# Kernel optimization log

Measured on AMD Instinct MI355X. Metric: run time of the kernel, lower is better.

## Reference

```python
import jax, jax.numpy as jnp
import numpy as np

B, T_IN, T_OUT, R = 32, 128, 500, 5
MEM_D, ATT, DEC, MEL, SPEC = 256, 256, 256, 128, 513
SPK_N, SPK_D = 5, 32
N_STYLE, STYLE_D, STYLE_ATT = 10, 2, 2
STEPS = T_OUT // R


def _gru(x, h, Wg, bg, Wc, bc):
    # TF GRUCell: r,u gates then candidate with reset-gated state
    gates = jax.nn.sigmoid(jnp.concatenate([x, h], -1) @ Wg + bg)
    r, u = jnp.split(gates, 2, axis=-1)
    c = jnp.tanh(jnp.concatenate([x, r * h], -1) @ Wc + bc)
    return u * h + (1.0 - u) * c


def setup_inputs() -> dict:
    key = jax.random.key(0)
    ks = iter(jax.random.split(key, 48))
    def nrm(shape, s=0.05):
        return (jax.random.normal(next(ks), shape) * s).astype(jnp.float32)
    return dict(
        encoder_output=nrm((B, T_IN, MEM_D), 1.0),
        style_token=nrm((N_STYLE, STYLE_D), 1.0),
        mel_gtruth=nrm((B, T_OUT, MEL), 1.0),
        speaker=jax.random.randint(next(ks), (B,), 0, SPK_N),
        inp_mask=jax.random.randint(next(ks), (B,), T_IN // 2, T_IN + 1),
        spk_embed=nrm((SPK_N, SPK_D)),
        Wp1=nrm((MEL, 256)), bp1=jnp.zeros((256,), jnp.float32),
        Wp2=nrm((256, 128)), bp2=jnp.zeros((128,), jnp.float32),
        Wg_att=nrm((128 + SPK_D + ATT, 2 * ATT)), bg_att=jnp.ones((2 * ATT,), jnp.float32),
        Wc_att=nrm((128 + SPK_D + ATT, ATT)), bc_att=jnp.zeros((ATT,), jnp.float32),
        Wk=nrm((MEM_D, ATT)), Wq=nrm((ATT, ATT)), v_att=nrm((ATT,)),
        Ws_pre=nrm((STYLE_D, STYLE_D)), bs_pre=jnp.zeros((STYLE_D,), jnp.float32),
        Wk_s=nrm((STYLE_D, STYLE_ATT)), Wq_s=nrm((ATT, STYLE_ATT)), v_s=nrm((STYLE_ATT,)),
        Wa=nrm((ATT + SPK_D + MEM_D + STYLE_D, DEC)), ba=jnp.zeros((DEC,), jnp.float32),
        Wg1=nrm((2 * DEC, 2 * DEC)), bg1=jnp.ones((2 * DEC,), jnp.float32),
        Wc1=nrm((2 * DEC, DEC)), bc1=jnp.zeros((DEC,), jnp.float32),
        Wg2=nrm((2 * DEC, 2 * DEC)), bg2=jnp.ones((2 * DEC,), jnp.float32),
        Wc2=nrm((2 * DEC, DEC)), bc2=jnp.zeros((DEC,), jnp.float32),
        Wo=nrm((DEC, MEL * R)), bo=jnp.zeros((MEL * R,), jnp.float32),
        Wspec=nrm((MEL, SPEC)), bspec=jnp.zeros((SPEC,), jnp.float32),
    )


def reference(encoder_output, style_token, mel_gtruth, speaker, inp_mask, spk_embed,
              Wp1, bp1, Wp2, bp2, Wg_att, bg_att, Wc_att, bc_att,
              Wk, Wq, v_att, Ws_pre, bs_pre, Wk_s, Wq_s, v_s,
              Wa, ba, Wg1, bg1, Wc1, bc1, Wg2, bg2, Wc2, bc2,
              Wo, bo, Wspec, bspec):
    mask = jnp.arange(T_IN)[None, :] < inp_mask[:, None]          # [B, T_in]
    keys = encoder_output @ Wk                                     # precomputed attention keys [B,T_in,ATT]
    spk = spk_embed[speaker]                                       # [B, 32]
    mem_style = jax.nn.relu(style_token @ Ws_pre + bs_pre)         # style pre-net [10, 2]
    keys_s = mem_style @ Wk_s                                      # [10, 2]
    # teacher forcing: frame fed at step t is indic[r*t + r - 1] = last gt frame of previous group
    mel_t = jnp.transpose(mel_gtruth, (1, 0, 2))                   # [T_out, B, MEL]
    last = mel_t[R - 1::R]                                         # [STEPS, B, MEL]
    prev = jnp.concatenate([jnp.zeros((1, B, MEL), mel_gtruth.dtype), last[:-1]], 0)

    def step(carry, frame):
        h_att, h1, h2 = carry
        # decoder pre-net (dropout disabled: is_training=False)
        p = jax.nn.relu(frame @ Wp1 + bp1)
        p = jax.nn.relu(p @ Wp2 + bp2)
        h_att = _gru(jnp.concatenate([p, spk], -1), h_att, Wg_att, bg_att, Wc_att, bc_att)
        q = h_att
        # content attention (Bahdanau) over encoder memory
        e = jnp.einsum('bta,a->bt', jnp.tanh(keys + (q @ Wq)[:, None, :]), v_att)
        alpha = jax.nn.softmax(jnp.where(mask, e, -1e9), axis=-1)
        context = jnp.einsum('bt,btd->bd', alpha, encoder_output)
        # style attention over 10 style tokens
        e_s = jnp.einsum('bna,a->bn', jnp.tanh(keys_s[None, :, :] + (q @ Wq_s)[:, None, :]), v_s)
        alpha_s = jax.nn.softmax(e_s, axis=-1)
        context_s = alpha_s @ mem_style                            # [B, 2]
        aco_in = jnp.concatenate([h_att, spk, context, context_s], -1) @ Wa + ba
        # two residual-wrapped GRU layers
        h1n = _gru(aco_in, h1, Wg1, bg1, Wc1, bc1)
        y1 = h1n + aco_in
        h2n = _gru(y1, h2, Wg2, bg2, Wc2, bc2)
        y2 = h2n + y1
        return (h_att, h1n, h2n), (y2 @ Wo + bo, alpha)

    init = (jnp.zeros((B, ATT), jnp.float32),
            jnp.zeros((B, DEC), jnp.float32),
            jnp.zeros((B, DEC), jnp.float32))
    _, (outs, alphas) = jax.lax.scan(step, init, prev)
    output_mel = jnp.transpose(outs, (1, 0, 2)).reshape(B, T_OUT, MEL)
    output_spec = output_mel @ Wspec + bspec
    final_alpha = jnp.transpose(alphas, (1, 0, 2))                 # [B, STEPS, T_in]
    return output_mel, output_spec, final_alpha
```

## Files before the change

### kernel.cpp

```cpp
#include <hip/hip_runtime.h>

typedef unsigned short ushort_t;
typedef unsigned int   uint_t;
typedef unsigned long long u64;
typedef __attribute__((ext_vector_type(8))) short  bf16x8;
typedef __attribute__((ext_vector_type(4))) float  f32x4;

#define B_      32
#define TIN_    128
#define TOUT_   500
#define R_      5
#define STEPS_  100
#define MEL_    128
#define SPEC_   513
#define NWG_    32

#define ZB_SLOTS   0
#define ZB_AH      8192
#define ZB_ARH     24576
#define ZB_AHC     40960
#define ZB_AXH1    73728
#define ZB_AXRH1   106496
#define ZB_AY1H2   139264
#define ZB_AY1RH2  172032
#define ZB_UBUF    221184
#define ZB_U1BUF   253952
#define ZB_U2BUF   286720
#define ZB_QSBUF   335872
#define ZB_END     435200
#define OFF_ACOSPK2 505856
#define OFF_MS2     538624
#define OFF_KS2     539136
#define OFF_SPK2    501760
#define OFF_PREG2   539648
#define OFF_PREC2   7093248
#define OFF_Y2G     10370048
#define OFF_KEYSP   13646848
#define OFF_ENCP    15744000
#define OFF_WQB     17841152

__device__ __forceinline__ float bf1(ushort_t u){ return __uint_as_float(((uint_t)u) << 16); }
__device__ __forceinline__ ushort_t f2bf(float f){
    uint_t b = __float_as_uint(f);
    uint_t r = (b + 0x7fffu + ((b >> 16) & 1u)) >> 16;
    return (ushort_t)r;
}
__device__ __forceinline__ float fexp2(float x){ return __builtin_amdgcn_exp2f(x); }
__device__ __forceinline__ float frcp(float x){ return __builtin_amdgcn_rcpf(x); }
__device__ __forceinline__ float sigm_f(float x){ return frcp(1.f + fexp2(-1.44269504f * x)); }
__device__ __forceinline__ float tanh_f(float x){
    float e = fexp2(2.88539008f * x);
    return 1.f - 2.f * frcp(e + 1.f);
}
__device__ __forceinline__ u64 ld8(const void* p){
    return __hip_atomic_load((const u64*)p, __ATOMIC_RELAXED, __HIP_MEMORY_SCOPE_AGENT);
}
__device__ __forceinline__ void st8(void* p, u64 v){
    __hip_atomic_store((u64*)p, v, __ATOMIC_RELAXED, __HIP_MEMORY_SCOPE_AGENT);
}
__device__ __forceinline__ float ld4f(const void* p){
    uint_t u = __hip_atomic_load((const uint_t*)p, __ATOMIC_RELAXED, __HIP_MEMORY_SCOPE_AGENT);
    return __uint_as_float(u);
}
__device__ __forceinline__ void st4f(void* p, float v){
    __hip_atomic_store((uint_t*)p, __float_as_uint(v), __ATOMIC_RELAXED, __HIP_MEMORY_SCOPE_AGENT);
}
__device__ __forceinline__ float u64lo(u64 v){ return __uint_as_float((uint_t)v); }
__device__ __forceinline__ float u64hi(u64 v){ return __uint_as_float((uint_t)(v >> 32)); }
__device__ __forceinline__ u64 pack4(const ushort_t* q){
    return (u64)q[0] | ((u64)q[1] << 16) | ((u64)q[2] << 32) | ((u64)q[3] << 48);
}
__device__ __forceinline__ u64 pack2f(const float* f){
    return (u64)__float_as_uint(f[0]) | ((u64)__float_as_uint(f[1]) << 32);
}
#define CBAR() asm volatile("" ::: "memory")

__global__ __launch_bounds__(256) void k_small(
    const float* __restrict__ st, const float* __restrict__ Ws_pre,
    const float* __restrict__ bs_pre, const float* __restrict__ Wk_s,
    const float* __restrict__ spk_embed, const int* __restrict__ speaker,
    const float* __restrict__ Wa, const float* __restrict__ ba,
    float* __restrict__ spk_sel, float* __restrict__ aco_spk,
    float* __restrict__ ms_g, float* __restrict__ ks_g)
{
    __shared__ float spk_l[B_*32];
    __shared__ float ms_l[20];
    const int tid = threadIdx.x;
    for(int i=tid; i<B_*32; i+=256){
        int b = i >> 5, j = i & 31;
        float v = spk_embed[speaker[b]*32 + j];
        spk_l[i] = v; spk_sel[i] = v;
    }
    if(tid < 20){
        int n = tid >> 1, j = tid & 1;
        float v = st[n*2]*Ws_pre[j] + st[n*2+1]*Ws_pre[2+j] + bs_pre[j];
        v = fmaxf(v, 0.f);
        ms_l[tid] = v; ms_g[tid] = v;
    }
    __syncthreads();
    if(tid < 20){
        int n = tid >> 1, j = tid & 1;
        ks_g[tid] = ms_l[n*2]*Wk_s[j] + ms_l[n*2+1]*Wk_s[2+j];
    }
    for(int i=tid; i<B_*256; i+=256){
        int b = i >> 8, n = i & 255;
        float acc = ba[n];
        #pragma unroll
        for(int k=0;k<32;++k) acc = fmaf(spk_l[b*32+k], Wa[(256+k)*256 + n], acc);
        aco_spk[i] = acc;
    }
}

__global__ __launch_bounds__(256) void k_keys(const float* __restrict__ enc,
                                              const float* __restrict__ Wk,
                                              ushort_t* __restrict__ keysb){
    __shared__ float x16[16][256];
    const int bid = blockIdx.x;
    const int b = bid >> 3, tg = bid & 7, t0 = tg*16;
    const int tid = threadIdx.x;
    for(int i=tid; i<16*256; i+=256){
        int r = i >> 8, k = i & 255;
        x16[r][k] = enc[((size_t)b*TIN_ + t0 + r)*256 + k];
    }
    __syncthreads();
    float acc[16];
    #pragma unroll
    for(int r=0;r<16;++r) acc[r] = 0.f;
    for(int k=0;k<256;++k){
        float w = Wk[k*256 + tid];
        #pragma unroll
        for(int r=0;r<16;++r) acc[r] = fmaf(x16[r][k], w, acc[r]);
    }
    #pragma unroll
    for(int r=0;r<16;++r)
        keysb[((size_t)b*TIN_ + t0 + r)*256 + tid] = f2bf(acc[r]);
}

__global__ __launch_bounds__(256) void k_cvt_enc(const float* __restrict__ enc,
                                                 ushort_t* __restrict__ encb){
    int o = blockIdx.x*256 + threadIdx.x;
    encb[o] = f2bf(enc[o]);
}
__global__ __launch_bounds__(256) void k_cvt_wq(const float* __restrict__ Wq,
                                                ushort_t* __restrict__ wqT){
    int o = blockIdx.x*256 + threadIdx.x;
    int k = o >> 8, c = o & 255;
    wqT[(k>>3)*2048 + c*8 + (k&7)] = f2bf(Wq[k*256 + c]);
}

__global__ __launch_bounds__(256) void k_prenet(
    const float* __restrict__ mg, const float* __restrict__ spk_sel,
    const float* __restrict__ Wp1, const float* __restrict__ bp1,
    const float* __restrict__ Wp2, const float* __restrict__ bp2,
    const float* __restrict__ Wg_att, const float* __restrict__ bg_att,
    const float* __restrict__ Wc_att, const float* __restrict__ bc_att,
    float* __restrict__ preg, float* __restrict__ prec)
{
    __shared__ float fr[16][128];
    __shared__ float p1[16][256];
    __shared__ float p2[16][128];
    __shared__ float spk_l[16][32];
    const int r0 = blockIdx.x * 16;
    const int tid = threadIdx.x;
    for(int i=tid; i<16*128; i+=256){
        int r = i >> 7, mcol = i & 127;
        int row = r0 + r, s = row >> 5, b = row & 31;
        fr[r][mcol] = (s == 0) ? 0.f : mg[((size_t)b*TOUT_ + s*R_ - 1)*MEL_ + mcol];
    }
    for(int i=tid; i<16*32; i+=256){
        int r = i >> 5, j = i & 31;
        spk_l[r][j] = spk_sel[((r0 + r) & 31)*32 + j];
    }
    __syncthreads();
    {
        float acc[16];
        #pragma unroll
        for(int r=0;r<16;++r) acc[r]=0.f;
        for(int k=0;k<128;++k){
            float w = Wp1[k*256 + tid];
            #pragma unroll
            for(int r=0;r<16;++r) acc[r] = fmaf(fr[r][k], w, acc[r]);
        }
        float bb = bp1[tid];
        #pragma unroll
        for(int r=0;r<16;++r) p1[r][tid] = fmaxf(acc[r] + bb, 0.f);
    }
    __syncthreads();
    if(tid < 128){
        float acc[16];
        #pragma unroll
        for(int r=0;r<16;++r) acc[r]=0.f;
        for(int k=0;k<256;++k){
            float w = Wp2[k*128 + tid];
            #pragma unroll
            for(int r=0;r<16;++r) acc[r] = fmaf(p1[r][k], w, acc[r]);
        }
        float bb = bp2[tid];
        #pragma unroll
        for(int r=0;r<16;++r) p2[r][tid] = fmaxf(acc[r] + bb, 0.f);
    }
    __syncthreads();
    {
        float aA[16], aB[16];
        #pragma unroll
        for(int r=0;r<16;++r){ aA[r]=0.f; aB[r]=0.f; }
        for(int k=0;k<128;++k){
            float wA = Wg_att[k*512 + tid], wB = Wg_att[k*512 + tid + 256];
            #pragma unroll
            for(int r=0;r<16;++r){ float pv = p2[r][k]; aA[r]=fmaf(pv,wA,aA[r]); aB[r]=fmaf(pv,wB,aB[r]); }
        }
        for(int k=0;k<32;++k){
            float wA = Wg_att[(128+k)*512 + tid], wB = Wg_att[(128+k)*512 + tid + 256];
            #pragma unroll
            for(int r=0;r<16;++r){ float sv = spk_l[r][k]; aA[r]=fmaf(sv,wA,aA[r]); aB[r]=fmaf(sv,wB,aB[r]); }
        }
        float bA = bg_att[tid], bB = bg_att[tid + 256];
        #pragma unroll
        for(int r=0;r<16;++r){
            preg[(size_t)(r0+r)*512 + tid]       = aA[r] + bA;
            preg[(size_t)(r0+r)*512 + tid + 256] = aB[r] + bB;
        }
    }
    {
        float acc[16];
        #pragma unroll
        for(int r=0;r<16;++r) acc[r]=0.f;
        for(int k=0;k<128;++k){
            float w = Wc_att[k*256 + tid];
            #pragma unroll
            for(int r=0;r<16;++r) acc[r] = fmaf(p2[r][k], w, acc[r]);
        }
        for(int k=0;k<32;++k){
            float w = Wc_att[(128+k)*256 + tid];
            #pragma unroll
            for(int r=0;r<16;++r) acc[r] = fmaf(spk_l[r][k], w, acc[r]);
        }
        float bb = bc_att[tid];
        #pragma unroll
        for(int r=0;r<16;++r) prec[(size_t)(r0+r)*256 + tid] = acc[r] + bb;
    }
}

__device__ __forceinline__ void gridbar(int* slots, int p, int seq, int tid){
    asm volatile("s_waitcnt vmcnt(0)" ::: "memory");
    __syncthreads();
    if(tid == 0)
        __hip_atomic_store(&slots[p*32], seq, __ATOMIC_RELEASE, __HIP_MEMORY_SCOPE_AGENT);
    if(tid < NWG_){
        while(__hip_atomic_load(&slots[tid*32], __ATOMIC_RELAXED, __HIP_MEMORY_SCOPE_AGENT) < seq)
            __builtin_amdgcn_s_sleep(1);
    }
    __syncthreads();
}

__device__ __forceinline__ void loadW(const float* W, int ldw, int rowbase, int nk, int kbase,
                                      int Ktot, int col0, int ncols, ushort_t* lds, int tid){
    for(int e = tid; e < 16*nk; e += 512){
        int col = e & 15, k = e >> 4;
        ushort_t v = 0;
        if(col < ncols) v = f2bf(W[(size_t)(rowbase + k)*ldw + col0 + col]);
        lds[(col*Ktot + kbase + k) ^ ((col & 7) << 3)] = v;
    }
}

template<int K>
__device__ __forceinline__ f32x4 do_gemm(const ushort_t* Ab, const ushort_t* Wl, float* red,
                                         int m, int kq, int lane){
    const int row = m*16 + (lane & 15);
    const int col = lane & 15;
    const int ko  = (lane >> 4) * 8;
    u64 av[K/64];
    #pragma unroll
    for(int t = 0; t < K/128; ++t){
        const int k0 = kq*(K/4) + t*32 + ko;
        av[2*t]   = ld8(Ab + row*K + k0);
        av[2*t+1] = ld8(Ab + row*K + k0 + 4);
    }
    f32x4 acc = {0.f,0.f,0.f,0.f};
    #pragma unroll
    for(int t = 0; t < K/128; ++t){
        const int k0 = kq*(K/4) + t*32 + ko;
        union { u64 q[2]; bf16x8 v; } ua;
        ua.q[0] = av[2*t]; ua.q[1] = av[2*t+1];
        bf16x8 b = *reinterpret_cast<const bf16x8*>(Wl + ((col*K + k0) ^ ((col & 7) << 3)));
        acc = __builtin_amdgcn_mfma_f32_16x16x32_bf16(ua.v, b, acc, 0, 0, 0);
    }
    if(kq > 0) *reinterpret_cast<f32x4*>(red + ((kq-1)*2 + m)*256 + lane*4) = acc;
    __syncthreads();
    if(kq == 0){
        #pragma unroll
        for(int j = 0; j < 3; ++j)
            acc += *reinterpret_cast<const f32x4*>(red + (j*2 + m)*256 + lane*4);
    }
    return acc;
}

__global__ __launch_bounds__(512) void k_scan_coop(
    char* ws,
    const float* __restrict__ Wg_att, const float* __restrict__ Wc_att,
    const float* __restrict__ Wq_s,
    const float* __restrict__ v_att, const float* __restrict__ v_s,
    const float* __restrict__ Wa,
    const float* __restrict__ Wg1, const float* __restrict__ Wc1,
    const float* __restrict__ Wg2, const float* __restrict__ Wc2,
    const float* __restrict__ bg1, const float* __restrict__ bc1,
    const float* __restrict__ bg2, const float* __restrict__ bc2,
    const int* __restrict__ inp_mask, float* __restrict__ out_alpha)
{
    const int p = blockIdx.x, tid = threadIdx.x;
    const int lane = tid & 63, wv = tid >> 6;
    const int m = wv & 1, kq = wv >> 1;

    int* slots       = (int*)(ws + ZB_SLOTS);
    ushort_t* A_h    = (ushort_t*)(ws + ZB_AH);
    ushort_t* A_rh   = (ushort_t*)(ws + ZB_ARH);
    ushort_t* A_hc   = (ushort_t*)(ws + ZB_AHC);
    ushort_t* A_xh1  = (ushort_t*)(ws + ZB_AXH1);
    ushort_t* A_xrh1 = (ushort_t*)(ws + ZB_AXRH1);
    ushort_t* A_y1h2 = (ushort_t*)(ws + ZB_AY1H2);
    ushort_t* A_y1rh2= (ushort_t*)(ws + ZB_AY1RH2);
    float* ubuf  = (float*)(ws + ZB_UBUF);
    float* u1buf = (float*)(ws + ZB_U1BUF);
    float* u2buf = (float*)(ws + ZB_U2BUF);
    float* qsbuf = (float*)(ws + ZB_QSBUF);
    const float* acospk = (const float*)(ws + OFF_ACOSPK2);
    const float* msg    = (const float*)(ws + OFF_MS2);
    const float* ksg    = (const float*)(ws + OFF_KS2);
    const float* preg   = (const float*)(ws + OFF_PREG2);
    const float* prec   = (const float*)(ws + OFF_PREC2);
    float* y2g          = (float*)(ws + OFF_Y2G);
    const ushort_t* keysb = (const ushort_t*)(ws + OFF_KEYSP);
    const ushort_t* encb  = (const ushort_t*)(ws + OFF_ENCP);
    const ushort_t* wqT   = (const ushort_t*)(ws + OFF_WQB);

    __shared__ ushort_t wA[16*256], wB[16*256];
    __shared__ ushort_t wG[16*512], wH[16*512], wI[16*512], wJ[16*512], wK[16*512];
    __shared__ __align__(16) char uni[16384];
    float* red = (float*)uni;
    float* uf  = (float*)uni;
    ushort_t* stg  = (ushort_t*)(uni + 8192);
    float*    stgf = (float*)(uni + 10240);
    __shared__ float vatt_l[256];
    __shared__ float msks[48];
    __shared__ float ctxs_l[64];
    __shared__ float acosl[256], acofl[256], y1fl[256];
    __shared__ float hfl[256], h1fl[256], h2fl[256];
    __shared__ float bg1s[16], bc1s[8], bg2s[16], bc2s[8], wasl[16];
    __shared__ float wqs_l[512];

    loadW(Wg_att, 512, 160, 256, 0, 256, p*16, 16, wA, tid);
    loadW(Wc_att, 256, 160, 256, 0, 256, p*8,  8,  wB, tid);
    loadW(Wa,     256, 0,   256, 0,   512, p*8, 8, wG, tid);
    loadW(Wa,     256, 288, 256, 256, 512, p*8, 8, wG, tid);
    loadW(Wg1,    512, 0,   512, 0, 512, p*16, 16, wH, tid);
    loadW(Wc1,    256, 0,   512, 0, 512, p*8,  8,  wI, tid);
    loadW(Wg2,    512, 0,   512, 0, 512, p*16, 16, wJ, tid);
    loadW(Wc2,    256, 0,   512, 0, 512, p*8,  8,  wK, tid);
    if(tid < 256){
        vatt_l[tid] = v_att[tid];
        acosl[tid]  = acospk[(tid>>3)*256 + p*8 + (tid&7)];
        hfl[tid] = 0.f; h1fl[tid] = 0.f; h2fl[tid] = 0.f;
    }
    wqs_l[tid] = Wq_s[tid];
    if(tid < 20) msks[tid] = msg[tid];
    if(tid >= 20 && tid < 40) msks[tid] = ksg[tid-20];
    if(tid == 40) msks[40] = v_s[0];
    if(tid == 41) msks[41] = v_s[1];
    if(tid < 16){ bg1s[tid] = bg1[p*16+tid]; bg2s[tid] = bg2[p*16+tid]; }
    if(tid < 8){ bc1s[tid] = bc1[p*8+tid]; bc2s[tid] = bc2[p*8+tid]; }
    if(tid < 16) wasl[tid] = Wa[(size_t)(544 + (tid & 1))*256 + p*8 + (tid >> 1)];
    const int maskp = inp_mask[p];
    __syncthreads();

    int seq = 0;
    for(int s = 0; s < STEPS_; ++s){
        const int sb = s*32;
        const int col = lane & 15;
        const int bbase = m*16 + ((lane>>4)<<2);
        __syncthreads();
        u64 hpre[4];
        if(kq == 0 && p < 16){
            #pragma unroll
            for(int r=0;r<4;++r) hpre[r] = ld8(A_h + (bbase+r)*256 + ((p*16+col) & ~3));
        }
        f32x4 acc = do_gemm<256>(A_h, wA, red, m, kq, lane);
        if(kq == 0){
            const int gcol = p*16 + col;
            if(p < 16){
                #pragma unroll
                for(int r=0;r<4;++r){
                    int b = bbase + r;
                    float g = sigm_f(acc[r] + preg[(size_t)(sb + b)*512 + gcol]);
                    float hb = bf1((ushort_t)(hpre[r] >> ((col & 3)*16)));
                    stg[b*16 + col] = f2bf(g * hb);
                }
                CBAR();
                int c = lane, row2 = m*16 + (c>>2), cg = c & 3;
                st8(A_rh + row2*256 + p*16 + cg*4, pack4(stg + row2*16 + cg*4));
            } else {
                #pragma unroll
                for(int r=0;r<4;++r){
                    int b = bbase + r;
                    stgf[b*16 + col] = sigm_f(acc[r] + preg[(size_t)(sb + b)*512 + gcol]);
                }
                CBAR();
                #pragma unroll
                for(int j=0;j<2;++j){
                    int c = lane*2 + j, row2 = m*16 + (c>>3), cg = c & 7;
                    st8(ubuf + row2*256 + (p-16)*16 + cg*2, pack2f(stgf + row2*16 + cg*2));
                }
            }
        }
        gridbar(slots, p, ++seq, tid);
        float upre[4];
        if(kq == 0 && col < 8){
            #pragma unroll
            for(int r=0;r<4;++r) upre[r] = ld4f(ubuf + (bbase+r)*256 + p*8 + col);
        }
        acc = do_gemm<256>(A_rh, wB, red, m, kq, lane);
        if(kq == 0){
            if(col < 8){
                const int gcol = p*8 + col;
                #pragma unroll
                for(int r=0;r<4;++r){
                    int b = bbase + r;
                    float cc = tanh_f(acc[r] + prec[(size_t)(sb + b)*256 + gcol]);
                    float u  = upre[r];
                    float hn = u*hfl[b*8 + col] + (1.f - u)*cc;
                    hfl[b*8 + col] = hn;
                    stg[b*8 + col] = f2bf(hn);
                }
            }
            CBAR();
            if(lane < 32){
                int c = lane, row2 = m*16 + (c>>1), cg = c & 1;
                u64 v = pack4(stg + row2*8 + cg*4);
                st8(A_h  + row2*256 + p*8 + cg*4, v);
                st8(A_hc + row2*512 + p*8 + cg*4, v);
            }
        }
        gridbar(slots, p, ++seq, tid);
        {
            float* hrow   = uf;
            float* qpart  = uf + 256;
            float* qrow   = uf + 768;
            float* escore = uf + 1024;
            float* alphaA = uf + 1152;
            float* smv    = uf + 1280;
            float* cpart  = uf + 1536;
            if(tid < 64){
                u64 h4 = ld8(A_h + p*256 + tid*4);
                #pragma unroll
                for(int j=0;j<4;++j) hrow[tid*4+j] = bf1((ushort_t)(h4 >> (j*16)));
            }
            __syncthreads();
            {
                int colq = tid & 255, kh = tid >> 8;
                const ushort_t* wq = wqT + kh*32768 + colq*8;
                float accq = 0.f;
                #pragma unroll 4
                for(int k8=0;k8<16;++k8){
                    bf16x8 w = *(const bf16x8*)(wq + k8*2048);
                    #pragma unroll
                    for(int j=0;j<8;++j)
                        accq = fmaf(hrow[kh*128 + k8*8 + j], bf1((ushort_t)w[j]), accq);
                }
                qpart[kh*256 + colq] = accq;
            }
            if(tid < 16){
                float q0s=0.f, q1s=0.f;
                #pragma unroll
                for(int kk=0;kk<16;++kk){
                    int k = tid*16 + kk; float hv = hrow[k];
                    q0s = fmaf(hv, wqs_l[k*2],   q0s);
                    q1s = fmaf(hv, wqs_l[k*2+1], q1s);
                }
                #pragma unroll
                for(int d=1; d<16; d<<=1){ q0s += __shfl_xor(q0s,d,64); q1s += __shfl_xor(q1s,d,64); }
                if(tid == 0){
                    float es[10]; float mx = -1e30f;
                    #pragma unroll
                    for(int n=0;n<10;++n){
                        float t = msks[40]*tanh_f(msks[20+n*2] + q0s) + msks[41]*tanh_f(msks[20+n*2+1] + q1s);
                        es[n] = t; mx = fmaxf(mx, t);
                    }
                    float sum = 0.f;
                    #pragma unroll
                    for(int n=0;n<10;++n){ float pe = fexp2((es[n]-mx)*1.44269504f); es[n]=pe; sum += pe; }
                    float inv = frcp(sum); float c0=0.f, c1=0.f;
                    #pragma unroll
                    for(int n=0;n<10;++n){ float al = es[n]*inv; c0 = fmaf(al, msks[n*2], c0); c1 = fmaf(al, msks[n*2+1], c1); }
                    float pr2[2] = {c0, c1};
                    st8(qsbuf + p*2, pack2f(pr2));
                }
            }
            __syncthreads();
            if(tid < 256) qrow[tid] = qpart[tid] + qpart[256+tid];
            __syncthreads();
            {
                int t = tid >> 2, q = tid & 3;
                const ushort_t* kp = keysb + ((size_t)(p*TIN_ + t))*256 + q*64;
                float e = 0.f;
                #pragma unroll
                for(int i2=0;i2<8;++i2){
                    bf16x8 kv = *(const bf16x8*)(kp + i2*8);
                    #pragma unroll
                    for(int j=0;j<8;++j){
                        int a = q*64 + i2*8 + j;
                        e = fmaf(vatt_l[a], tanh_f(bf1((ushort_t)kv[j]) + qrow[a]), e);
                    }
                }
                e += __shfl_xor(e,1,64); e += __shfl_xor(e,2,64);
                if(q == 0) escore[t] = (t < maskp) ? e : -1e9f;
            }
            __syncthreads();
            if(tid < 64){
                float e0 = escore[tid], e1 = escore[tid+64];
                float mx = fmaxf(e0, e1);
                #pragma unroll
                for(int d=1; d<64; d<<=1) mx = fmaxf(mx, __shfl_xor(mx,d,64));
                float a0 = fexp2((e0-mx)*1.44269504f);
                float a1 = fexp2((e1-mx)*1.44269504f);
                alphaA[tid] = a0; alphaA[tid+64] = a1;
                float ssum = a0 + a1;
                #pragma unroll
                for(int d=1; d<64; d<<=1) ssum += __shfl_xor(ssum,d,64);
                if(tid == 0) smv[0] = frcp(ssum);
            }
            __syncthreads();
            if(tid < 128){
                float a = alphaA[tid] * smv[0];
                alphaA[tid] = a;
                st4f(out_alpha + ((size_t)p*STEPS_ + s)*TIN_ + tid, a);
            }
            __syncthreads();
            {
                int colq = tid & 255, th = tid >> 8;
                const ushort_t* ep = encb + ((size_t)(p*TIN_ + th*64))*256 + colq;
                float c = 0.f;
                #pragma unroll 4
                for(int tt=0; tt<64; ++tt) c = fmaf(alphaA[th*64+tt], bf1(ep[(size_t)tt*256]), c);
                cpart[th*256 + colq] = c;
            }
            __syncthreads();
            if(tid < 256) stg[tid] = f2bf(cpart[tid] + cpart[256+tid]);
            CBAR();
            __syncthreads();
            if(tid < 64) st8(A_hc + p*512 + 256 + tid*4, pack4(stg + tid*4));
        }
        gridbar(slots, p, ++seq, tid);
        if(tid < 32){
            u64 qq = ld8(qsbuf + tid*2);
            ctxs_l[tid*2] = u64lo(qq); ctxs_l[tid*2+1] = u64hi(qq);
        }
        acc = do_gemm<512>(A_hc, wG, red, m, kq, lane);
        if(kq == 0){
            if(col < 8){
                #pragma unroll
                for(int r=0;r<4;++r){
                    int b = bbase + r;
                    float v = acc[r] + acosl[b*8 + col]
                            + ctxs_l[b*2]   * wasl[col*2]
                            + ctxs_l[b*2+1] * wasl[col*2+1];
                    acofl[b*8 + col] = v;
                    stg[b*8 + col] = f2bf(v);
                }
            }
            CBAR();
            if(lane < 32){
                int c = lane, row2 = m*16 + (c>>1), cg = c & 1;
                u64 v = pack4(stg + row2*8 + cg*4);
                st8(A_xh1  + row2*512 + p*8 + cg*4, v);
                st8(A_xrh1 + row2*512 + p*8 + cg*4, v);
            }
        }
        gridbar(slots, p, ++seq, tid);
        if(kq == 0 && p < 16){
            #pragma unroll
            for(int r=0;r<4;++r) hpre[r] = ld8(A_xh1 + (bbase+r)*512 + 256 + ((p*16+col) & ~3));
        }
        acc = do_gemm<512>(A_xh1, wH, red, m, kq, lane);
        if(kq == 0){
            if(p < 16){
                #pragma unroll
                for(int r=0;r<4;++r){
                    int b = bbase + r;
                    float g = sigm_f(acc[r] + bg1s[col]);
                    float hb = bf1((ushort_t)(hpre[r] >> ((col & 3)*16)));
                    stg[b*16 + col] = f2bf(g * hb);
                }
                CBAR();
                int c = lane, row2 = m*16 + (c>>2), cg = c & 3;
                st8(A_xrh1 + row2*512 + 256 + p*16 + cg*4, pack4(stg + row2*16 + cg*4));
            } else {
                #pragma unroll
                for(int r=0;r<4;++r)
                    stgf[(bbase+r)*16 + col] = sigm_f(acc[r] + bg1s[col]);
                CBAR();
                #pragma unroll
                for(int j=0;j<2;++j){
                    int c = lane*2 + j, row2 = m*16 + (c>>3), cg = c & 7;
                    st8(u1buf + row2*256 + (p-16)*16 + cg*2, pack2f(stgf + row2*16 + cg*2));
                }
            }
        }
        gridbar(slots, p, ++seq, tid);
        if(kq == 0 && col < 8){
            #pragma unroll
            for(int r=0;r<4;++r) upre[r] = ld4f(u1buf + (bbase+r)*256 + p*8 + col);
        }
        acc = do_gemm<512>(A_xrh1, wI, red, m, kq, lane);
        if(kq == 0){
            if(col < 8){
                #pragma unroll
                for(int r=0;r<4;++r){
                    int b = bbase + r;
                    float cc = tanh_f(acc[r] + bc1s[col]);
                    float u  = upre[r];
                    float hn = u*h1fl[b*8 + col] + (1.f - u)*cc;
                    h1fl[b*8 + col] = hn;
                    stg[b*8 + col] = f2bf(hn);
                    float y1 = hn + acofl[b*8 + col];
                    y1fl[b*8 + col] = y1;
                    stg[256 + b*8 + col] = f2bf(y1);
                }
            }
            CBAR();
            if(lane < 32){
                int c = lane, row2 = m*16 + (c>>1), cg = c & 1;
                u64 vh = pack4(stg + row2*8 + cg*4);
                u64 vy = pack4(stg + 256 + row2*8 + cg*4);
                st8(A_xh1   + row2*512 + 256 + p*8 + cg*4, vh);
                st8(A_y1h2  + row2*512 + p*8 + cg*4, vy);
                st8(A_y1rh2 + row2*512 + p*8 + cg*4, vy);
            }
        }
        gridbar(slots, p, ++seq, tid);
        if(kq == 0 && p < 16){
            #pragma unroll
            for(int r=0;r<4;++r) hpre[r] = ld8(A_y1h2 + (bbase+r)*512 + 256 + ((p*16+col) & ~3));
        }
        acc = do_gemm<512>(A_y1h2, wJ, red, m, kq, lane);
        if(kq == 0){
            if(p < 16){
                #pragma unroll
                for(int r=0;r<4;++r){
                    int b = bbase + r;
                    float g = sigm_f(acc[r] + bg2s[col]);
                    float hb = bf1((ushort_t)(hpre[r] >> ((col & 3)*16)));
                    stg[b*16 + col] = f2bf(g * hb);
                }
                CBAR();
                int c = lane, row2 = m*16 + (c>>2), cg = c & 3;
                st8(A_y1rh2 + row2*512 + 256 + p*16 + cg*4, pack4(stg + row2*16 + cg*4));
            } else {
                #pragma unroll
                for(int r=0;r<4;++r)
                    stgf[(bbase+r)*16 + col] = sigm_f(acc[r] + bg2s[col]);
                CBAR();
                #pragma unroll
                for(int j=0;j<2;++j){
                    int c = lane*2 + j, row2 = m*16 + (c>>3), cg = c & 7;
                    st8(u2buf + row2*256 + (p-16)*16 + cg*2, pack2f(stgf + row2*16 + cg*2));
                }
            }
        }
        gridbar(slots, p, ++seq, tid);
        if(kq == 0 && col < 8){
            #pragma unroll
            for(int r=0;r<4;++r) upre[r] = ld4f(u2buf + (bbase+r)*256 + p*8 + col);
        }
        acc = do_gemm<512>(A_y1rh2, wK, red, m, kq, lane);
        if(kq == 0){
            if(col < 8){
                const int gcol = p*8 + col;
                #pragma unroll
                for(int r=0;r<4;++r){
                    int b = bbase + r;
                    float cc = tanh_f(acc[r] + bc2s[col]);
                    float u  = upre[r];
                    float hn = u*h2fl[b*8 + col] + (1.f - u)*cc;
                    h2fl[b*8 + col] = hn;
                    stg[b*8 + col] = f2bf(hn);
                    st4f(y2g + ((size_t)sb + b)*256 + gcol, hn + y1fl[b*8 + col]);
                }
            }
            CBAR();
            if(lane < 32){
                int c = lane, row2 = m*16 + (c>>1), cg = c & 1;
                st8(A_y1h2 + row2*512 + 256 + p*8 + cg*4, pack4(stg + row2*8 + cg*4));
            }
        }
    }
}

__global__ __launch_bounds__(256) void k_omel(const float* __restrict__ y2g,
                                              const float* __restrict__ Wo,
                                              const float* __restrict__ bo,
                                              float* __restrict__ out_mel){
    __shared__ float y8[8][256];
    const int r0 = blockIdx.x * 8;
    const int tid = threadIdx.x;
    for(int i=tid; i<8*256; i+=256){ int r=i>>8, k=i&255; y8[r][k] = y2g[(size_t)(r0+r)*256 + k]; }
    __syncthreads();
    float aA[8], aB[8], aC[8];
    #pragma unroll
    for(int r=0;r<8;++r){ aA[r]=0.f; aB[r]=0.f; aC[r]=0.f; }
    for(int k=0;k<256;++k){
        float wA = Wo[(size_t)k*640 + tid];
        float wB = Wo[(size_t)k*640 + tid + 256];
        float wC = (tid < 128) ? Wo[(size_t)k*640 + tid + 512] : 0.f;
        #pragma unroll
        for(int r=0;r<8;++r){
            float yv = y8[r][k];
            aA[r]=fmaf(yv,wA,aA[r]); aB[r]=fmaf(yv,wB,aB[r]); aC[r]=fmaf(yv,wC,aC[r]);
        }
    }
    float bA = bo[tid], bB = bo[tid+256], bC = (tid<128)? bo[tid+512] : 0.f;
    #pragma unroll
    for(int r=0;r<8;++r){
        int row = r0 + r, s = row >> 5, b = row & 31;
        int mm = tid & 127;
        out_mel[((size_t)b*TOUT_ + s*R_ + (tid>>7))*MEL_ + mm]     = aA[r] + bA;
        out_mel[((size_t)b*TOUT_ + s*R_ + 2 + (tid>>7))*MEL_ + mm] = aB[r] + bB;
        if(tid < 128)
            out_mel[((size_t)b*TOUT_ + s*R_ + 4)*MEL_ + tid]       = aC[r] + bC;
    }
}

__global__ __launch_bounds__(256) void k_spec(const float* __restrict__ out_mel,
                                              const float* __restrict__ Wspec,
                                              const float* __restrict__ bspec,
                                              float* __restrict__ out_spec){
    __shared__ float m8[8][128];
    const int r0 = blockIdx.x * 8;
    const int tid = threadIdx.x;
    for(int i=tid; i<8*128; i+=256){ int r=i>>7, k=i&127; m8[r][k] = out_mel[(size_t)(r0+r)*128 + k]; }
    __syncthreads();
    float aA[8], aB[8], aC[8];
    #pragma unroll
    for(int r=0;r<8;++r){ aA[r]=0.f; aB[r]=0.f; aC[r]=0.f; }
    for(int k=0;k<128;++k){
        float wA = Wspec[(size_t)k*SPEC_ + tid];
        float wB = Wspec[(size_t)k*SPEC_ + 256 + tid];
        float wC = (tid == 0) ? Wspec[(size_t)k*SPEC_ + 512] : 0.f;
        #pragma unroll
        for(int r=0;r<8;++r){
            float mv = m8[r][k];
            aA[r]=fmaf(mv,wA,aA[r]); aB[r]=fmaf(mv,wB,aB[r]); aC[r]=fmaf(mv,wC,aC[r]);
        }
    }
    float bA = bspec[tid], bB = bspec[256+tid];
    #pragma unroll
    for(int r=0;r<8;++r){
        size_t row = (size_t)(r0 + r);
        out_spec[row*SPEC_ + tid]       = aA[r] + bA;
        out_spec[row*SPEC_ + 256 + tid] = aB[r] + bB;
        if(tid == 0) out_spec[row*SPEC_ + 512] = aC[r] + bspec[512];
    }
}

extern "C" void kernel_launch(void* const* d_in, const int* in_sizes, int n_in,
                              void* d_out, int out_size, void* d_ws, size_t ws_size,
                              hipStream_t stream) {
    const float* enc       = (const float*)d_in[0];
    const float* st        = (const float*)d_in[1];
    const float* mg        = (const float*)d_in[2];
    const int*   speaker   = (const int*)  d_in[3];
    const int*   inp_mask  = (const int*)  d_in[4];
    const float* spk_embed = (const float*)d_in[5];
    const float* Wp1=(const float*)d_in[6],  *bp1=(const float*)d_in[7];
    const float* Wp2=(const float*)d_in[8],  *bp2=(const float*)d_in[9];
    const float* Wg_att=(const float*)d_in[10], *bg_att=(const float*)d_in[11];
    const float* Wc_att=(const float*)d_in[12], *bc_att=(const float*)d_in[13];
    const float* Wk=(const float*)d_in[14], *Wq=(const float*)d_in[15], *v_att=(const float*)d_in[16];
    const float* Ws_pre=(const float*)d_in[17], *bs_pre=(const float*)d_in[18];
    const float* Wk_s=(const float*)d_in[19], *Wq_s=(const float*)d_in[20], *v_s=(const float*)d_in[21];
    const float* Wa=(const float*)d_in[22], *ba=(const float*)d_in[23];
    const float* Wg1=(const float*)d_in[24], *bg1=(const float*)d_in[25];
    const float* Wc1=(const float*)d_in[26], *bc1=(const float*)d_in[27];
    const float* Wg2=(const float*)d_in[28], *bg2=(const float*)d_in[29];
    const float* Wc2=(const float*)d_in[30], *bc2=(const float*)d_in[31];
    const float* Wo=(const float*)d_in[32], *bo=(const float*)d_in[33];
    const float* Wspec=(const float*)d_in[34], *bspec=(const float*)d_in[35];

    float* out       = (float*)d_out;
    float* out_mel   = out;
    float* out_spec  = out + 2048000;
    float* out_alpha = out + 10256000;

    char* ws = (char*)d_ws;
    float*    spk_sel = (float*)(ws + OFF_SPK2);
    float*    aco_spk = (float*)(ws + OFF_ACOSPK2);
    float*    ms_g    = (float*)(ws + OFF_MS2);
    float*    ks_g    = (float*)(ws + OFF_KS2);
    float*    preg    = (float*)(ws + OFF_PREG2);
    float*    prec    = (float*)(ws + OFF_PREC2);
    float*    y2g     = (float*)(ws + OFF_Y2G);
    ushort_t* keysb   = (ushort_t*)(ws + OFF_KEYSP);
    ushort_t* encb    = (ushort_t*)(ws + OFF_ENCP);
    ushort_t* wqT     = (ushort_t*)(ws + OFF_WQB);

    hipMemsetAsync(d_ws, 0, ZB_END, stream);

    k_small<<<dim3(1), dim3(256), 0, stream>>>(st, Ws_pre, bs_pre, Wk_s, spk_embed,
                                               speaker, Wa, ba, spk_sel, aco_spk, ms_g, ks_g);
    k_keys   <<<dim3(256),  dim3(256), 0, stream>>>(enc, Wk, keysb);
    k_cvt_enc<<<dim3(4096), dim3(256), 0, stream>>>(enc, encb);
    k_cvt_wq <<<dim3(256),  dim3(256), 0, stream>>>(Wq, wqT);
    k_prenet <<<dim3(200),  dim3(256), 0, stream>>>(mg, spk_sel, Wp1, bp1, Wp2, bp2,
                                                    Wg_att, bg_att, Wc_att, bc_att, preg, prec);
    k_scan_coop<<<dim3(NWG_), dim3(512), 0, stream>>>(ws, Wg_att, Wc_att, Wq_s,
                                                      v_att, v_s, Wa, Wg1, Wc1, Wg2, Wc2,
                                                      bg1, bc1, bg2, bc2, inp_mask, out_alpha);
    k_omel <<<dim3(400),  dim3(256), 0, stream>>>(y2g, Wo, bo, out_mel);
    k_spec <<<dim3(2000), dim3(256), 0, stream>>>(out_mel, Wspec, bspec, out_spec);
}
```

Before: 3.792 ms.

## Fold Wa into GRU1 gate weights to remove one grid barrier per step

Precomputes Wa·Wg1 (the input half), the speaker/bias term and the style-context rows on the device, so the first GRU's gate preactivation can be computed directly from the attention output in the same phase as aco_in. This removes one dependent GEMM phase and one grid-wide barrier from each of the 100 sequential decoder steps. In exchange it adds two small prep kernels, extra per-step GEMMs with extra __syncthreads, and rounding differs because the product weight is quantised to bf16.

```diff
diff --git a/kernel.cpp b/kernel.cpp
--- a/kernel.cpp
+++ b/kernel.cpp
@@ -38,6 +38,9 @@
 #define OFF_KEYSP   13646848
 #define OFF_ENCP    15744000
 #define OFF_WQB     17841152
+#define OFF_WAG     17972224
+#define OFF_ACOS1   19020800
+#define OFF_WSG     19086336
 
 __device__ __forceinline__ float bf1(ushort_t u){ return __uint_as_float(((uint_t)u) << 16); }
 __device__ __forceinline__ ushort_t f2bf(float f){
@@ -108,6 +111,74 @@
         #pragma unroll
         for(int k=0;k<32;++k) acc = fmaf(spk_l[b*32+k], Wa[(256+k)*256 + n], acc);
         aco_spk[i] = acc;
+    }
+}
+
+__global__ __launch_bounds__(256) void k_prepA(const float* __restrict__ Wa,
+                                               const float* __restrict__ Wg1,
+                                               float* __restrict__ Wag){
+    __shared__ float aw[8][256];
+    const int r0 = blockIdx.x * 8;
+    const int tid = threadIdx.x;
+    for(int i=tid; i<8*256; i+=256){
+        int r = i >> 8, j = i & 255;
+        int k = r0 + r;
+        int row = (k < 256) ? k : 288 + (k - 256);
+        aw[r][j] = Wa[(size_t)row*256 + j];
+    }
+    __syncthreads();
+    float a0[8], a1[8];
+    #pragma unroll
+    for(int r=0;r<8;++r){ a0[r]=0.f; a1[r]=0.f; }
+    for(int j=0;j<256;++j){
+        float w0 = Wg1[(size_t)j*512 + tid];
+        float w1 = Wg1[(size_t)j*512 + 256 + tid];
+        #pragma unroll
+        for(int r=0;r<8;++r){ float av = aw[r][j]; a0[r]=fmaf(av,w0,a0[r]); a1[r]=fmaf(av,w1,a1[r]); }
+    }
+    #pragma unroll
+    for(int r=0;r<8;++r){
+        Wag[(size_t)(r0+r)*512 + tid]       = a0[r];
+        Wag[(size_t)(r0+r)*512 + 256 + tid] = a1[r];
+    }
+}
+
+__global__ __launch_bounds__(256) void k_prepB(const float* __restrict__ acospk,
+                                               const float* __restrict__ Wa,
+                                               const float* __restrict__ Wg1,
+                                               const float* __restrict__ bg1,
+                                               float* __restrict__ acospk1,
+                                               float* __restrict__ Wsg){
+    __shared__ float aw[8][256];
+    const int blk = blockIdx.x;
+    const int tid = threadIdx.x;
+    const int nrows = (blk < 4) ? 8 : 2;
+    const int r0 = blk * 8;
+    for(int i=tid; i<nrows*256; i+=256){
+        int r = i >> 8, j = i & 255;
+        aw[r][j] = (blk < 4) ? acospk[(size_t)(r0+r)*256 + j]
+                             : Wa[(size_t)(544+r)*256 + j];
+    }
+    __syncthreads();
+    float a0[8], a1[8];
+    #pragma unroll
+    for(int r=0;r<8;++r){ a0[r]=0.f; a1[r]=0.f; }
+    for(int j=0;j<256;++j){
+        float w0 = Wg1[(size_t)j*512 + tid];
+        float w1 = Wg1[(size_t)j*512 + 256 + tid];
+        for(int r=0;r<nrows;++r){ float av = aw[r][j]; a0[r]=fmaf(av,w0,a0[r]); a1[r]=fmaf(av,w1,a1[r]); }
+    }
+    if(blk < 4){
+        float b0 = bg1[tid], b1 = bg1[256+tid];
+        for(int r=0;r<8;++r){
+            acospk1[(size_t)(r0+r)*512 + tid]       = a0[r] + b0;
+            acospk1[(size_t)(r0+r)*512 + 256 + tid] = a1[r] + b1;
+        }
+    } else {
+        for(int r=0;r<2;++r){
+            Wsg[(size_t)r*512 + tid]       = a0[r];
+            Wsg[(size_t)r*512 + 256 + tid] = a1[r];
+        }
     }
 }
 
@@ -263,7 +334,7 @@
     }
 }
 
-template<int K>
+template<int K, int LDA = K>
 __device__ __forceinline__ f32x4 do_gemm(const ushort_t* Ab, const ushort_t* Wl, float* red,
                                          int m, int kq, int lane){
     const int row = m*16 + (lane & 15);
@@ -273,8 +344,8 @@
     #pragma unroll
     for(int t = 0; t < K/128; ++t){
         const int k0 = kq*(K/4) + t*32 + ko;
-        av[2*t]   = ld8(Ab + row*K + k0);
-        av[2*t+1] = ld8(Ab + row*K + k0 + 4);
+        av[2*t]   = ld8(Ab + row*LDA + k0);
+        av[2*t+1] = ld8(Ab + row*LDA + k0 + 4);
     }
     f32x4 acc = {0.f,0.f,0.f,0.f};
     #pragma unroll
@@ -303,7 +374,7 @@
     const float* __restrict__ Wa,
     const float* __restrict__ Wg1, const float* __restrict__ Wc1,
     const float* __restrict__ Wg2, const float* __restrict__ Wc2,
-    const float* __restrict__ bg1, const float* __restrict__ bc1,
+    const float* __restrict__ bc1,
     const float* __restrict__ bg2, const float* __restrict__ bc2,
     const int* __restrict__ inp_mask, float* __restrict__ out_alpha)
 {
@@ -332,9 +403,13 @@
     const ushort_t* keysb = (const ushort_t*)(ws + OFF_KEYSP);
     const ushort_t* encb  = (const ushort_t*)(ws + OFF_ENCP);
     const ushort_t* wqT   = (const ushort_t*)(ws + OFF_WQB);
+    const float* Wag      = (const float*)(ws + OFF_WAG);
+    const float* acospk1  = (const float*)(ws + OFF_ACOS1);
+    const float* Wsg      = (const float*)(ws + OFF_WSG);
 
     __shared__ ushort_t wA[16*256], wB[16*256];
-    __shared__ ushort_t wG[16*512], wH[16*512], wI[16*512], wJ[16*512], wK[16*512];
+    __shared__ ushort_t wG[16*512], wAG[16*512], wH1h[16*256];
+    __shared__ ushort_t wI[16*512], wJ[16*512], wK[16*512];
     __shared__ __align__(16) char uni[16384];
     float* red = (float*)uni;
     float* uf  = (float*)uni;
@@ -344,15 +419,18 @@
     __shared__ float msks[48];
     __shared__ float ctxs_l[64];
     __shared__ float acosl[256], acofl[256], y1fl[256];
+    __shared__ float acos1l[512];
+    __shared__ float wsg_l[32];
     __shared__ float hfl[256], h1fl[256], h2fl[256];
-    __shared__ float bg1s[16], bc1s[8], bg2s[16], bc2s[8], wasl[16];
+    __shared__ float bc1s[8], bg2s[16], bc2s[8], wasl[16];
     __shared__ float wqs_l[512];
 
     loadW(Wg_att, 512, 160, 256, 0, 256, p*16, 16, wA, tid);
     loadW(Wc_att, 256, 160, 256, 0, 256, p*8,  8,  wB, tid);
     loadW(Wa,     256, 0,   256, 0,   512, p*8, 8, wG, tid);
     loadW(Wa,     256, 288, 256, 256, 512, p*8, 8, wG, tid);
-    loadW(Wg1,    512, 0,   512, 0, 512, p*16, 16, wH, tid);
+    loadW(Wag,    512, 0,   512, 0, 512, p*16, 16, wAG, tid);
+    loadW(Wg1,    512, 256, 256, 0, 256, p*16, 16, wH1h, tid);
     loadW(Wc1,    256, 0,   512, 0, 512, p*8,  8,  wI, tid);
     loadW(Wg2,    512, 0,   512, 0, 512, p*16, 16, wJ, tid);
     loadW(Wc2,    256, 0,   512, 0, 512, p*8,  8,  wK, tid);
@@ -361,12 +439,14 @@
         acosl[tid]  = acospk[(tid>>3)*256 + p*8 + (tid&7)];
         hfl[tid] = 0.f; h1fl[tid] = 0.f; h2fl[tid] = 0.f;
     }
+    acos1l[tid] = acospk1[(size_t)(tid>>4)*512 + p*16 + (tid&15)];
     wqs_l[tid] = Wq_s[tid];
+    if(tid < 32) wsg_l[tid] = Wsg[(size_t)(tid>>4)*512 + p*16 + (tid&15)];
     if(tid < 20) msks[tid] = msg[tid];
     if(tid >= 20 && tid < 40) msks[tid] = ksg[tid-20];
     if(tid == 40) msks[40] = v_s[0];
     if(tid == 41) msks[41] = v_s[1];
-    if(tid < 16){ bg1s[tid] = bg1[p*16+tid]; bg2s[tid] = bg2[p*16+tid]; }
+    if(tid < 16) bg2s[tid] = bg2[p*16+tid];
     if(tid < 8){ bc1s[tid] = bc1[p*8+tid]; bc2s[tid] = bc2[p*8+tid]; }
     if(tid < 16) wasl[tid] = Wa[(size_t)(544 + (tid & 1))*256 + p*8 + (tid >> 1)];
     const int maskp = inp_mask[p];
@@ -553,7 +633,16 @@
             u64 qq = ld8(qsbuf + tid*2);
             ctxs_l[tid*2] = u64lo(qq); ctxs_l[tid*2+1] = u64hi(qq);
         }
+        u64 h1pre[4];
+        if(kq == 0 && p < 16){
+            #pragma unroll
+            for(int r=0;r<4;++r) h1pre[r] = ld8(A_xh1 + (bbase+r)*512 + 256 + ((p*16+col) & ~3));
+        }
         acc = do_gemm<512>(A_hc, wG, red, m, kq, lane);
+        __syncthreads();
+        f32x4 g1a = do_gemm<512>(A_hc, wAG, red, m, kq, lane);
+        __syncthreads();
+        f32x4 g1b = do_gemm<256,512>(A_xh1 + 256, wH1h, red, m, kq, lane);
         if(kq == 0){
             if(col < 8){
                 #pragma unroll
@@ -566,6 +655,25 @@
                     stg[b*8 + col] = f2bf(v);
                 }
             }
+            if(p < 16){
+                #pragma unroll
+                for(int r=0;r<4;++r){
+                    int b = bbase + r;
+                    float g = sigm_f(g1a[r] + g1b[r] + acos1l[b*16 + col]
+                                     + ctxs_l[b*2]   * wsg_l[col]
+                                     + ctxs_l[b*2+1] * wsg_l[16 + col]);
+                    float h1b = bf1((ushort_t)(h1pre[r] >> ((col & 3)*16)));
+                    stg[512 + b*16 + col] = f2bf(g * h1b);
+                }
+            } else {
+                #pragma unroll
+                for(int r=0;r<4;++r){
+                    int b = bbase + r;
+                    stgf[b*16 + col] = sigm_f(g1a[r] + g1b[r] + acos1l[b*16 + col]
+                                              + ctxs_l[b*2]   * wsg_l[col]
+                                              + ctxs_l[b*2+1] * wsg_l[16 + col]);
+                }
+            }
             CBAR();
             if(lane < 32){
                 int c = lane, row2 = m*16 + (c>>1), cg = c & 1;
@@ -573,30 +681,10 @@
                 st8(A_xh1  + row2*512 + p*8 + cg*4, v);
                 st8(A_xrh1 + row2*512 + p*8 + cg*4, v);
             }
-        }
-        gridbar(slots, p, ++seq, tid);
-        if(kq == 0 && p < 16){
-            #pragma unroll
-            for(int r=0;r<4;++r) hpre[r] = ld8(A_xh1 + (bbase+r)*512 + 256 + ((p*16+col) & ~3));
-        }
-        acc = do_gemm<512>(A_xh1, wH, red, m, kq, lane);
-        if(kq == 0){
             if(p < 16){
-                #pragma unroll
-                for(int r=0;r<4;++r){
-                    int b = bbase + r;
-                    float g = sigm_f(acc[r] + bg1s[col]);
-                    float hb = bf1((ushort_t)(hpre[r] >> ((col & 3)*16)));
-                    stg[b*16 + col] = f2bf(g * hb);
-                }
-                CBAR();
                 int c = lane, row2 = m*16 + (c>>2), cg = c & 3;
-                st8(A_xrh1 + row2*512 + 256 + p*16 + cg*4, pack4(stg + row2*16 + cg*4));
+                st8(A_xrh1 + row2*512 + 256 + p*16 + cg*4, pack4(stg + 512 + row2*16 + cg*4));
             } else {
-                #pragma unroll
-                for(int r=0;r<4;++r)
-                    stgf[(bbase+r)*16 + col] = sigm_f(acc[r] + bg1s[col]);
-                CBAR();
                 #pragma unroll
                 for(int j=0;j<2;++j){
                     int c = lane*2 + j, row2 = m*16 + (c>>3), cg = c & 7;
@@ -800,11 +888,16 @@
     ushort_t* keysb   = (ushort_t*)(ws + OFF_KEYSP);
     ushort_t* encb    = (ushort_t*)(ws + OFF_ENCP);
     ushort_t* wqT     = (ushort_t*)(ws + OFF_WQB);
+    float*    Wag     = (float*)(ws + OFF_WAG);
+    float*    acospk1 = (float*)(ws + OFF_ACOS1);
+    float*    Wsg     = (float*)(ws + OFF_WSG);
 
     hipMemsetAsync(d_ws, 0, ZB_END, stream);
 
     k_small<<<dim3(1), dim3(256), 0, stream>>>(st, Ws_pre, bs_pre, Wk_s, spk_embed,
                                                speaker, Wa, ba, spk_sel, aco_spk, ms_g, ks_g);
+    k_prepA<<<dim3(64), dim3(256), 0, stream>>>(Wa, Wg1, Wag);
+    k_prepB<<<dim3(5),  dim3(256), 0, stream>>>(aco_spk, Wa, Wg1, bg1, acospk1, Wsg);
     k_keys   <<<dim3(256),  dim3(256), 0, stream>>>(enc, Wk, keysb);
     k_cvt_enc<<<dim3(4096), dim3(256), 0, stream>>>(enc, encb);
     k_cvt_wq <<<dim3(256),  dim3(256), 0, stream>>>(Wq, wqT);
@@ -812,7 +905,7 @@
                                                     Wg_att, bg_att, Wc_att, bc_att, preg, prec);
     k_scan_coop<<<dim3(NWG_), dim3(512), 0, stream>>>(ws, Wg_att, Wc_att, Wq_s,
                                                       v_att, v_s, Wa, Wg1, Wc1, Wg2, Wc2,
-                                                      bg1, bc1, bg2, bc2, inp_mask, out_alpha);
+                                                      bc1, bg2, bc2, inp_mask, out_alpha);
     k_omel <<<dim3(400),  dim3(256), 0, stream>>>(y2g, Wo, bo, out_mel);
     k_spec <<<dim3(2000), dim3(256), 0, stream>>>(out_mel, Wspec, bspec, out_spec);
 }
```

After: 4.051 ms. +6.8%, slower.
